# Performance work log

Hardware: AMD Instinct MI355X
Metric: run time of the kernel (lower is better)

Reference implementation:

```python
import jax, jax.numpy as jnp
import numpy as np

D_MODEL = 1024
D_INNER = 2048      # expand * d_model
D_STATE = 64
HEADDIM = 128
NHEADS = 16         # d_inner // headdim
D_CONV = 4
CHUNK = 256
D_IN_PROJ = 2 * D_INNER + 2 * D_STATE + NHEADS   # 4240 (ngroups=1)
CONV_DIM = D_INNER + 2 * D_STATE                 # 2176
EPS = 1e-5


def setup_inputs() -> dict:
    key = jax.random.key(0)
    ks = jax.random.split(key, 8)
    B, L = 2, 4096
    u = jax.random.normal(ks[0], (B, L, D_MODEL), jnp.float32)
    in_proj_w = jax.random.normal(ks[1], (D_IN_PROJ, D_MODEL), jnp.float32) / np.sqrt(D_MODEL)
    conv_w = jax.random.uniform(ks[2], (CONV_DIM, D_CONV), jnp.float32, -0.5, 0.5)
    conv_b = jnp.zeros((CONV_DIM,), jnp.float32)
    # dt_bias init exactly as in the module: inv-softplus of dt ~ logU(1e-3, 1e-1)
    dt0 = jnp.exp(jax.random.uniform(ks[3], (NHEADS,), jnp.float32) * (np.log(0.1) - np.log(0.001)) + np.log(0.001))
    dt_bias = dt0 + jnp.log(-jnp.expm1(-dt0))
    A_log = jnp.log(jax.random.uniform(ks[4], (NHEADS,), jnp.float32, 1.0, 16.0))
    Dp = jnp.ones((NHEADS,), jnp.float32)
    norm_w = jnp.ones((D_INNER,), jnp.float32)
    out_proj_w = jax.random.normal(ks[5], (D_MODEL, D_INNER), jnp.float32) / np.sqrt(D_INNER)
    return dict(u=u, in_proj_w=in_proj_w, conv_w=conv_w, conv_b=conv_b, dt_bias=dt_bias,
                A_log=A_log, Dp=Dp, norm_w=norm_w, out_proj_w=out_proj_w)


def _ssd(x, dt, A, Bm, Cm, Dp):
    # Chunked selective state-space scan (mamba_chunk_scan_combined semantics).
    # x: [b,l,h,p], dt: [b,l,h] (already softplus'd), A: [h] (negative), Bm/Cm: [b,l,n]
    b, l, h, p = x.shape
    n = Bm.shape[-1]
    nc = l // CHUNK
    xc = x.reshape(b, nc, CHUNK, h, p)
    dtc = dt.reshape(b, nc, CHUNK, h)
    Bc = Bm.reshape(b, nc, CHUNK, n)
    Cc = Cm.reshape(b, nc, CHUNK, n)
    a = dtc * A                       # [b,c,q,h], a <= 0
    acum = jnp.cumsum(a, axis=2)      # within-chunk cumulative log-decay
    # ---- intra-chunk (causal, attention-like) ----
    scores = jnp.einsum('bcqn,bckn->bcqk', Cc, Bc)
    diff = acum[:, :, :, None, :] - acum[:, :, None, :, :]        # [b,c,q,k,h]
    mask = jnp.tril(jnp.ones((CHUNK, CHUNK), bool))[None, None, :, :, None]
    decay = jnp.exp(jnp.where(mask, diff, -jnp.inf))
    M = scores[..., None] * decay * dtc[:, :, None, :, :]         # [b,c,q,k,h]
    y_diag = jnp.einsum('bcqkh,bckhp->bcqhp', M, xc)
    # ---- per-chunk end states ----
    decay_states = jnp.exp(acum[:, :, -1:, :] - acum)             # [b,c,q,h]
    states = jnp.einsum('bcqh,bcqn,bcqhp->bchpn', dtc * decay_states, Bc, xc)
    # ---- inter-chunk recurrence (scan over nc chunks) ----
    chunk_decay = jnp.exp(acum[:, :, -1, :])                      # [b,c,h]
    def step(s, inp):
        st, cd = inp
        return cd[:, :, None, None] * s + st, s                   # emit state BEFORE this chunk
    init = jnp.zeros((b, h, p, n), x.dtype)
    _, prev = jax.lax.scan(step, init, (states.transpose(1, 0, 2, 3, 4), chunk_decay.transpose(1, 0, 2)))
    prev = prev.transpose(1, 0, 2, 3, 4)                          # [b,c,h,p,n]
    y_off = jnp.einsum('bcqn,bchpn,bcqh->bcqhp', Cc, prev, jnp.exp(acum))
    y = y_diag + y_off + xc * Dp[None, None, None, :, None]
    return y.reshape(b, l, h, p)


def _forward(u, in_proj_w, conv_w, conv_b, dt_bias, A_log, Dp, norm_w, out_proj_w):
    b, l, _ = u.shape
    zxbct = jnp.einsum('bld,ed->ble', u, in_proj_w)
    z = zxbct[..., :D_INNER]
    xBC = zxbct[..., D_INNER:D_INNER + CONV_DIM]
    dt = zxbct[..., D_INNER + CONV_DIM:]
    dt = jax.nn.softplus(dt + dt_bias)                            # [b,l,h]
    # causal depthwise conv1d (padding d_conv-1, truncated to seq_len) + SiLU
    xp = jnp.pad(xBC, ((0, 0), (D_CONV - 1, 0), (0, 0)))
    conv_out = conv_b
    for w in range(D_CONV):
        conv_out = conv_out + xp[:, w:w + l, :] * conv_w[:, w]
    xBC = jax.nn.silu(conv_out)
    x = xBC[..., :D_INNER]
    Bm = xBC[..., D_INNER:D_INNER + D_STATE]
    Cm = xBC[..., D_INNER + D_STATE:]
    A = -jnp.exp(A_log)
    y = _ssd(x.reshape(b, l, NHEADS, HEADDIM), dt, A, Bm, Cm, Dp)
    y = y.reshape(b, l, D_INNER)
    # RMSNormGated (norm_before_gate=False): gate first, then RMSNorm
    y = y * jax.nn.silu(z)
    y = y * jax.lax.rsqrt(jnp.mean(y * y, axis=-1, keepdims=True) + EPS) * norm_w
    return jnp.einsum('ble,de->bld', y, out_proj_w)


def reference(u, in_proj_w, conv_w, conv_b, dt_bias, A_log, Dp, norm_w, out_proj_w):
    return _forward(u, in_proj_w, conv_w, conv_b, dt_bias, A_log, Dp, norm_w, out_proj_w)
```

## Files before the change

kernel.cpp:

```cpp
#include <hip/hip_runtime.h>
#include <hip/hip_bf16.h>
#include <cstdint>
#include <cstddef>

#define D_MODEL   1024
#define D_INNER   2048
#define D_STATE   64
#define HEADDIM   128
#define NHEADS    16
#define D_CONV    4
#define CHUNK     256
#define D_IN_PROJ 4240
#define ZPAD      4352
#define CONV_DIM  2176
#define NB        2
#define LEN       4096
#define NC        16
#define MROWS     (NB*LEN)

typedef __hip_bfloat16 bf16;
typedef __bf16 bf16x8 __attribute__((ext_vector_type(8)));
typedef float  f32x4  __attribute__((ext_vector_type(4)));
typedef unsigned short us4 __attribute__((ext_vector_type(4)));

__device__ __forceinline__ float fsilu(float x){ return x / (1.f + __expf(-x)); }
__device__ __forceinline__ float toF(float x){ return x; }
__device__ __forceinline__ float toF(bf16 x){ return __bfloat162float(x); }
__device__ __forceinline__ void storeF(float* p, float v){ *p = v; }
__device__ __forceinline__ void storeF(bf16* p, float v){ *p = __float2bfloat16(v); }

__device__ __forceinline__ unsigned short f2bs(float v){
  return __bfloat16_as_ushort(__float2bfloat16(v));
}
__device__ __forceinline__ void store4(bf16* p, f32x4 v){
  us4 o; o[0]=f2bs(v[0]); o[1]=f2bs(v[1]); o[2]=f2bs(v[2]); o[3]=f2bs(v[3]);
  *(us4*)p = o;
}
__device__ __forceinline__ void store4(float* p, f32x4 v){
  *(f32x4*)p = v;
}

__device__ __forceinline__ void gload_lds16(const void* g, void* l){
  __builtin_amdgcn_global_load_lds(
     (const __attribute__((address_space(1))) unsigned int*)(uintptr_t)g,
     (__attribute__((address_space(3))) unsigned int*)(uintptr_t)l, 16, 0, 0);
}

template<typename TC>
__global__ __launch_bounds__(512) void k_gemm_pipe(
    const bf16* __restrict__ A, int lda,
    const bf16* __restrict__ B, int ldb,
    TC* __restrict__ C, int ldc, int K)
{
  __shared__ __align__(16) char lds[3*49152];
  const int tid  = threadIdx.x;
  const int w    = tid >> 6, l = tid & 63;
  const int quad = l >> 4, lq = l & 15;
  const int wm   = w >> 1, wn = w & 1;

  const int nwg  = gridDim.x;
  const int orig = blockIdx.x;
  const int wg   = (orig & 7)*(nwg >> 3) + (orig >> 3);
  const int m0   = (wg & 31)*256;
  const int n0   = (wg >> 5)*128;

  const int rs = tid >> 3;
  const int cs = ((tid & 7) ^ (rs & 7)) * 8;
  const bf16* Ag = A + (size_t)(m0 + rs)*lda + cs;
  const bf16* Bg = B + (size_t)(n0 + rs)*ldb + cs;
  const int sdo = w*1024;

  auto stage = [&](int k0, char* bufb){
    #pragma unroll
    for (int p=0;p<4;p++)
      gload_lds16(Ag + (size_t)p*64*lda + k0, bufb + sdo + p*8192);
    #pragma unroll
    for (int p=0;p<2;p++)
      gload_lds16(Bg + (size_t)p*64*ldb + k0, bufb + 32768 + sdo + p*8192);
  };

  char* bufA = lds;
  char* bufB = lds + 49152;
  char* bufC = lds + 98304;

  f32x4 acc[4][4] = {};
  const int sl0 = (quad ^ (lq & 7)) * 16;
  const int sl1 = sl0 ^ 64;
  const int aro = (wm*64 + lq)*128;
  const int bro = 32768 + (wn*64 + lq)*128;

  stage(0,  bufA);
  stage(64, bufB);
  asm volatile("s_waitcnt vmcnt(6)" ::: "memory");
  __builtin_amdgcn_s_barrier();
  asm volatile("" ::: "memory");

  const int NT = K >> 6;
  for (int t = 0; t < NT; ++t){
    if (t + 2 < NT) stage((t+2) << 6, bufC);

    bf16x8 af[2][4], bfr[2][4];
    #pragma unroll
    for (int m=0;m<4;m++){
      af[0][m]  = *(const bf16x8*)(bufA + aro + m*2048 + sl0);
      af[1][m]  = *(const bf16x8*)(bufA + aro + m*2048 + sl1);
      bfr[0][m] = *(const bf16x8*)(bufA + bro + m*2048 + sl0);
      bfr[1][m] = *(const bf16x8*)(bufA + bro + m*2048 + sl1);
    }
    __builtin_amdgcn_s_setprio(1);
    #pragma unroll
    for (int ks=0;ks<2;ks++)
      #pragma unroll
      for (int m=0;m<4;m++)
        #pragma unroll
        for (int n=0;n<4;n++)
          acc[m][n] = __builtin_amdgcn_mfma_f32_16x16x32_bf16(bfr[ks][n], af[ks][m], acc[m][n], 0,0,0);
    __builtin_amdgcn_s_setprio(0);

    __builtin_amdgcn_sched_barrier(0);
    if (t == NT-2) { asm volatile("s_waitcnt vmcnt(0)" ::: "memory"); }
    else           { asm volatile("s_waitcnt vmcnt(6)" ::: "memory"); }
    __builtin_amdgcn_s_barrier();
    asm volatile("" ::: "memory");
    char* tmp = bufA; bufA = bufB; bufB = bufC; bufC = tmp;
  }

  #pragma unroll
  for (int m=0;m<4;m++){
    const int r = m0 + wm*64 + m*16 + lq;
    #pragma unroll
    for (int n=0;n<4;n++){
      const int cb = n0 + wn*64 + n*16 + quad*4;
      store4(&C[(size_t)r*ldc + cb], acc[m][n]);
    }
  }
}

#define NU4  (MROWS*D_MODEL/4)
#define NW14 (ZPAD*D_MODEL/4)
#define NW24 (D_MODEL*D_INNER/4)
__global__ __launch_bounds__(256) void k_convert(
    const float* __restrict__ u, const float* __restrict__ Win,
    const float* __restrict__ Wout, const float* __restrict__ norm_w,
    bf16* __restrict__ ub, bf16* __restrict__ Wb_in, bf16* __restrict__ Wb_out){
  int i4 = blockIdx.x*256 + threadIdx.x;
  if (i4 < NU4){
    float4 v = ((const float4*)u)[i4];
    us4 o = {f2bs(v.x), f2bs(v.y), f2bs(v.z), f2bs(v.w)};
    ((us4*)ub)[i4] = o;
  } else if (i4 < NU4 + NW14){
    int j = i4 - NU4;
    int r = j >> 8;
    float4 v = make_float4(0.f,0.f,0.f,0.f);
    if (r < D_IN_PROJ) v = ((const float4*)Win)[j];
    us4 o = {f2bs(v.x), f2bs(v.y), f2bs(v.z), f2bs(v.w)};
    ((us4*)Wb_in)[j] = o;
  } else {
    int j = i4 - NU4 - NW14;
    float4 v = ((const float4*)Wout)[j];
    float4 nw = ((const float4*)norm_w)[j & 511];
    us4 o = {f2bs(v.x*nw.x), f2bs(v.y*nw.y), f2bs(v.z*nw.z), f2bs(v.w*nw.w)};
    ((us4*)Wb_out)[j] = o;
  }
}

__global__ __launch_bounds__(256) void k_dt(
    const bf16* __restrict__ zxbct, const float* __restrict__ dt_bias,
    const float* __restrict__ A_log, float* __restrict__ dt_t,
    float* __restrict__ acum_t, float* __restrict__ cd_t){
  int bid = blockIdx.x;
  int h = bid & 15, c = (bid>>4)&15, b = bid>>8;
  int q = threadIdx.x;
  size_t m = (size_t)(b*NC + c)*CHUNK + q;
  float x = toF(zxbct[m*ZPAD + (D_INNER + CONV_DIM) + h]) + dt_bias[h];
  float dtv = (x > 20.f) ? x : log1pf(__expf(x));
  float Ah = -__expf(A_log[h]);
  float a = dtv * Ah;
  __shared__ float sb[CHUNK];
  sb[q] = a;
  __syncthreads();
  #pragma unroll
  for (int off=1; off<CHUNK; off<<=1){
    float t = (q >= off) ? sb[q-off] : 0.f;
    __syncthreads();
    sb[q] += t;
    __syncthreads();
  }
  float ac = sb[q];
  size_t o = ((size_t)(b*NHEADS+h))*LEN + c*CHUNK + q;
  dt_t[o]   = dtv;
  acum_t[o] = ac;
  if (q == CHUNK-1) cd_t[(b*NHEADS+h)*NC + c] = __expf(ac);
}

__global__ __launch_bounds__(256) void k_conv(
    const bf16* __restrict__ zxbct, const float* __restrict__ conv_w,
    const float* __restrict__ conv_b, bf16* __restrict__ xbc){
  __shared__ __align__(16) __bf16 xs[67*64];
  __shared__ __align__(16) float  ws[64*4];
  __shared__ float bs[64];
  const int tid = threadIdx.x;
  const int cq = tid & 7;
  const int tm = tid >> 3;
  const int c0 = blockIdx.x*64;
  const int m0 = blockIdx.y*64;
  {
    int g = m0 - 3 + tm; if (g < 0) g = 0;
    *(bf16x8*)&xs[tm*64 + cq*8] =
        *(const bf16x8*)(zxbct + (size_t)g*ZPAD + D_INNER + c0 + cq*8);
    int g2 = m0 - 3 + tm + 32;
    *(bf16x8*)&xs[(tm+32)*64 + cq*8] =
        *(const bf16x8*)(zxbct + (size_t)g2*ZPAD + D_INNER + c0 + cq*8);
    if (tid < 24){
      int r3 = 64 + (tid >> 3);
      int g3 = m0 - 3 + r3;
      *(bf16x8*)&xs[r3*64 + cq*8] =
          *(const bf16x8*)(zxbct + (size_t)g3*ZPAD + D_INNER + c0 + cq*8);
    }
  }
  if (tid < 64)      *(float4*)&ws[tid*4] = *(const float4*)(conv_w + (size_t)(c0+tid)*4);
  else if (tid < 128) bs[tid-64] = conv_b[c0 + tid - 64];
  __syncthreads();

  #pragma unroll
  for (int rr=0; rr<2; rr++){
    const int r = tm + rr*32;
    const int m = m0 + r;
    const int l = m & (LEN-1);
    float acc[8];
    #pragma unroll
    for (int j=0;j<8;j++) acc[j] = bs[cq*8+j];
    #pragma unroll
    for (int w=0; w<D_CONV; w++){
      if (l - (D_CONV-1) + w >= 0){
        bf16x8 v = *(const bf16x8*)&xs[(r+w)*64 + cq*8];
        #pragma unroll
        for (int j=0;j<8;j++) acc[j] += (float)v[j] * ws[(cq*8+j)*4 + w];
      }
    }
    bf16x8 o;
    #pragma unroll
    for (int j=0;j<8;j++) o[j] = (__bf16)fsilu(acc[j]);
    *(bf16x8*)(xbc + (size_t)m*CONV_DIM + c0 + cq*8) = o;
  }
}

__global__ __launch_bounds__(256,2) void k_states(
    const bf16* __restrict__ xbc, const float* __restrict__ acum_t,
    const float* __restrict__ dt_t, float* __restrict__ states)
{
  const int bid = blockIdx.x;
  const int h = bid & 15, c = (bid>>4)&15, b = bid>>8;
  const int z = b*NC + c;
  const int tid = threadIdx.x;
  const int w = tid >> 6, l = tid & 63;
  const int quad = l >> 4, lq = l & 15;

  __shared__ __align__(16) __bf16 xsT[2][128*72];
  __shared__ __align__(16) __bf16 bts[2][64*72];

  const float* acum = acum_t + ((size_t)(b*NHEADS+h))*LEN + c*CHUNK;
  const float* dtc  = dt_t   + ((size_t)(b*NHEADS+h))*LEN + c*CHUNK;
  const float alast = acum[CHUNK-1];
  const bf16* xrow = xbc + (size_t)z*CHUNK*CONV_DIM + h*HEADDIM;
  const bf16* Brow = xbc + (size_t)z*CHUNK*CONV_DIM + D_INNER;

  f32x4 Sst[2][4] = {};

  auto stage = [&](int t, int buf){
    const int k0 = t*64;
    const bf16* xr = xrow + (size_t)(k0+l)*CONV_DIM;
    #pragma unroll
    for (int pass=0; pass<4; pass++){
      int pb = w*8 + pass*32;
      bf16x8 v = *(const bf16x8*)(xr + pb);
      #pragma unroll
      for (int j=0;j<8;j++) xsT[buf][(pb+j)*72 + l] = v[j];
    }
    float wl = dtc[k0+l] * __expf(alast - acum[k0+l]);
    const bf16* br = Brow + (size_t)(k0+l)*CONV_DIM;
    #pragma unroll
    for (int pass=0; pass<2; pass++){
      int nb = w*8 + pass*32;
      bf16x8 v = *(const bf16x8*)(br + nb);
      #pragma unroll
      for (int j=0;j<8;j++) bts[buf][(nb+j)*72 + l] = (__bf16)((float)v[j] * wl);
    }
  };

  stage(0, 0);
  for (int t = 0; t < 4; t++){
    const int buf = t & 1;
    __syncthreads();
    if (t < 3) stage(t+1, buf^1);
    #pragma unroll
    for (int s=0;s<2;s++){
      bf16x8 a2[2];
      #pragma unroll
      for (int mi=0;mi<2;mi++)
        a2[mi] = *(const bf16x8*)&xsT[buf][(w*32 + mi*16 + lq)*72 + s*32 + quad*8];
      #pragma unroll
      for (int ni=0;ni<4;ni++){
        bf16x8 bb = *(const bf16x8*)&bts[buf][(ni*16+lq)*72 + s*32 + quad*8];
        #pragma unroll
        for (int mi=0;mi<2;mi++)
          Sst[mi][ni] = __builtin_amdgcn_mfma_f32_16x16x32_bf16(bb, a2[mi], Sst[mi][ni], 0,0,0);
      }
    }
  }

  float* so = states + (size_t)bid*HEADDIM*D_STATE;
  #pragma unroll
  for (int mi=0;mi<2;mi++){
    int pp = w*32 + mi*16 + lq;
    #pragma unroll
    for (int ni=0;ni<4;ni++)
      store4(&so[pp*D_STATE + ni*16 + quad*4], Sst[mi][ni]);
  }
}

__global__ __launch_bounds__(256) void k_scan(
    const float* __restrict__ states, const float* __restrict__ cd_t,
    bf16* __restrict__ prevb){
  int b = blockIdx.x >> 4, h = blockIdx.x & 15;
  int pt = blockIdx.y;
  int tid = threadIdx.x;
  float carry[4] = {0.f,0.f,0.f,0.f};
  for (int c=0;c<NC;c++){
    size_t base = ((size_t)(b*256 + c*16 + h))*HEADDIM*D_STATE + (size_t)pt*1024;
    float cd = cd_t[(b*NHEADS+h)*NC + c];
    #pragma unroll
    for (int i=0;i<4;i++){
      size_t idx = base + (size_t)i*256 + tid;
      prevb[idx] = __float2bfloat16(carry[i]);
      carry[i] = carry[i]*cd + states[idx];
    }
  }
}

__global__ __launch_bounds__(256,2) void k_fused(
    const bf16* __restrict__ xbc, const float* __restrict__ acum_t,
    const float* __restrict__ dt_t, const float* __restrict__ Dp,
    const bf16* __restrict__ prevb, bf16* __restrict__ y)
{
  const int bid = blockIdx.x;
  const int h = bid & 15, c = (bid>>4)&15, b = bid>>8;
  const int z = b*NC + c;
  const int tid = threadIdx.x;
  const int w = tid >> 6, l = tid & 63;
  const int quad = l >> 4, lq = l & 15;

  __shared__ __align__(16) __bf16 xsT[2][128*72];
  __shared__ __align__(16) __bf16 Ms[4][32*40];
  __shared__ float acs[CHUNK], dts[CHUNK];

  const float* acum = acum_t + ((size_t)(b*NHEADS+h))*LEN + c*CHUNK;
  const float* dtc  = dt_t   + ((size_t)(b*NHEADS+h))*LEN + c*CHUNK;
  acs[tid] = acum[tid];
  dts[tid] = dtc[tid];

  const bf16* xrow = xbc + (size_t)z*CHUNK*CONV_DIM + h*HEADDIM;
  const bf16* Brow = xbc + (size_t)z*CHUNK*CONV_DIM + D_INNER;
  const bf16* Crow = xbc + (size_t)z*CHUNK*CONV_DIM + D_INNER + D_STATE;
  const bf16* pv   = prevb + (size_t)bid*HEADDIM*D_STATE;
  const float Dph = Dp[h];
  const int j0 = w, j1 = 7 - w;

  f32x4 Yacc[2][2][8] = {};

  auto stage = [&](int t, int buf){
    const bf16* xr = xrow + (size_t)(t*64+l)*CONV_DIM;
    #pragma unroll
    for (int pass=0; pass<4; pass++){
      int pb = w*8 + pass*32;
      bf16x8 v = *(const bf16x8*)(xr + pb);
      #pragma unroll
      for (int j=0;j<8;j++) xsT[buf][(pb+j)*72 + l] = v[j];
    }
  };

  stage(0, 0);
  __syncthreads();

  #pragma unroll
  for (int s=0;s<2;s++){
    bf16x8 bp[8];
    #pragma unroll
    for (int pn=0;pn<8;pn++)
      bp[pn] = *(const bf16x8*)(pv + (pn*16+lq)*D_STATE + s*32 + quad*8);
    #pragma unroll
    for (int half=0; half<2; half++){
      const int j = half ? j1 : j0;
      #pragma unroll
      for (int qm=0;qm<2;qm++){
        int row = j*32 + qm*16 + lq;
        float e = __expf(acs[row]);
        bf16x8 a = *(const bf16x8*)(Crow + (size_t)row*CONV_DIM + s*32 + quad*8);
        bf16x8 ae;
        #pragma unroll
        for (int jj=0;jj<8;jj++) ae[jj] = (__bf16)((float)a[jj] * e);
        #pragma unroll
        for (int pn=0;pn<8;pn++)
          Yacc[half][qm][pn] = __builtin_amdgcn_mfma_f32_16x16x32_bf16(bp[pn], ae, Yacc[half][qm][pn], 0,0,0);
      }
    }
  }

  for (int t = 0; t < 4; t++){
    const int buf = t & 1;
    if (t > 0) __syncthreads();
    if (t < 3) stage(t+1, buf^1);

    #pragma unroll
    for (int half=0; half<2; half++){
      const int j = half ? j1 : j0;
      if (2*t > j) continue;
      const int qbase = j*32;
      bf16x8 cf[2][2];
      #pragma unroll
      for (int s=0;s<2;s++)
        #pragma unroll
        for (int qm=0;qm<2;qm++)
          cf[s][qm] = *(const bf16x8*)(Crow + (size_t)(qbase+qm*16+lq)*CONV_DIM + s*32 + quad*8);
      #pragma unroll
      for (int kk=0; kk<2; kk++){
        const int kh = 2*t + kk;
        if (kh > j) continue;
        const int kb32  = kk*32;
        const int kbase = kh*32;
        f32x4 Sacc[2][2] = {};
        #pragma unroll
        for (int s=0;s<2;s++){
          bf16x8 bfk[2];
          #pragma unroll
          for (int kn=0;kn<2;kn++)
            bfk[kn] = *(const bf16x8*)(Brow + (size_t)(kbase+kn*16+lq)*CONV_DIM + s*32 + quad*8);
          #pragma unroll
          for (int kn=0;kn<2;kn++)
            #pragma unroll
            for (int qm=0;qm<2;qm++)
              Sacc[kn][qm] = __builtin_amdgcn_mfma_f32_16x16x32_bf16(bfk[kn], cf[s][qm], Sacc[kn][qm], 0,0,0);
        }
        #pragma unroll
        for (int qm=0;qm<2;qm++){
          int ql = qbase + qm*16 + lq;
          float aq = acs[ql];
          #pragma unroll
          for (int kn=0;kn<2;kn++){
            us4 o;
            #pragma unroll
            for (int i=0;i<4;i++){
              int kl = kbase + kn*16 + quad*4 + i;
              float v = Sacc[kn][qm][i] * __expf(aq - acs[kl]) * dts[kl];
              v = (kl < ql) ? v : ((kl == ql) ? v + Dph : 0.f);
              o[i] = f2bs(v);
            }
            *(us4*)&Ms[w][(qm*16+lq)*40 + kn*16 + quad*4] = o;
          }
        }
        asm volatile("s_waitcnt lgkmcnt(0)" ::: "memory");
        #pragma unroll
        for (int qm=0;qm<2;qm++){
          bf16x8 am = *(const bf16x8*)&Ms[w][(qm*16+lq)*40 + quad*8];
          #pragma unroll
          for (int pn=0;pn<8;pn++){
            bf16x8 bp = *(const bf16x8*)&xsT[buf][(pn*16+lq)*72 + kb32 + quad*8];
            Yacc[half][qm][pn] = __builtin_amdgcn_mfma_f32_16x16x32_bf16(bp, am, Yacc[half][qm][pn], 0,0,0);
          }
        }
      }
    }
  }

  bf16* yrow = y + (size_t)z*CHUNK*D_INNER + h*HEADDIM;
  #pragma unroll
  for (int half=0; half<2; half++){
    const int j = half ? j1 : j0;
    #pragma unroll
    for (int qm=0;qm<2;qm++){
      int q = j*32 + qm*16 + lq;
      #pragma unroll
      for (int pn=0;pn<8;pn++)
        store4(&yrow[(size_t)q*D_INNER + pn*16 + quad*4], Yacc[half][qm][pn]);
    }
  }
}

__global__ __launch_bounds__(256) void k_gatenorm(
    const bf16* __restrict__ zxbct, bf16* __restrict__ y){
  int m = blockIdx.x;
  int e0 = threadIdx.x*8;
  bf16x8 zv = *(const bf16x8*)(zxbct + (size_t)m*ZPAD + e0);
  bf16x8 yv = *(const bf16x8*)(y + (size_t)m*D_INNER + e0);
  float v[8]; float ss = 0.f;
  #pragma unroll
  for (int j=0;j<8;j++){
    float val = (float)yv[j] * fsilu((float)zv[j]);
    v[j] = val; ss += val*val;
  }
  #pragma unroll
  for (int off=32; off>0; off>>=1) ss += __shfl_down(ss, off, 64);
  __shared__ float red[4];
  if ((threadIdx.x & 63) == 0) red[threadIdx.x >> 6] = ss;
  __syncthreads();
  float tot = red[0]+red[1]+red[2]+red[3];
  float r = rsqrtf(tot * (1.f/D_INNER) + 1e-5f);
  bf16x8 o;
  #pragma unroll
  for (int j=0;j<8;j++) o[j] = (__bf16)(v[j] * r);
  *(bf16x8*)(y + (size_t)m*D_INNER + e0) = o;
}

extern "C" void kernel_launch(void* const* d_in, const int* in_sizes, int n_in,
                              void* d_out, int out_size, void* d_ws, size_t ws_size,
                              hipStream_t stream) {
  const float* u         = (const float*)d_in[0];
  const float* in_proj_w = (const float*)d_in[1];
  const float* conv_w    = (const float*)d_in[2];
  const float* conv_b    = (const float*)d_in[3];
  const float* dt_bias   = (const float*)d_in[4];
  const float* A_log     = (const float*)d_in[5];
  const float* Dp        = (const float*)d_in[6];
  const float* norm_w    = (const float*)d_in[7];
  const float* out_proj_w= (const float*)d_in[8];
  float* out = (float*)d_out;

  char* p = (char*)d_ws;
  auto alloc = [&](size_t bytes){ char* r = p; p += (bytes + 255) & ~size_t(255); return r; };
  bf16*  zxbct = (bf16*) alloc((size_t)MROWS*ZPAD*2);
  bf16*  xbc   = (bf16*) alloc((size_t)MROWS*CONV_DIM*2);
  bf16*  y     = (bf16*) alloc((size_t)MROWS*D_INNER*2);
  bf16*  ub    = (bf16*) alloc((size_t)MROWS*D_MODEL*2);
  bf16*  Wb_in = (bf16*) alloc((size_t)ZPAD*D_MODEL*2);
  bf16*  Wb_out= (bf16*) alloc((size_t)D_MODEL*D_INNER*2);
  float* dt_t  = (float*)alloc((size_t)NB*NHEADS*LEN*4);
  float* acum_t= (float*)alloc((size_t)NB*NHEADS*LEN*4);
  float* cd_t  = (float*)alloc((size_t)NB*NHEADS*NC*4);
  float* states= (float*)ub;
  bf16*  prevb = (bf16*)Wb_in;

  dim3 blk(256);
  k_convert<<<dim3((NU4+NW14+NW24)/256), blk, 0, stream>>>(
      u, in_proj_w, out_proj_w, norm_w, ub, Wb_in, Wb_out);

  k_gemm_pipe<bf16><<<dim3(32*34), dim3(512), 0, stream>>>(
      ub, D_MODEL, Wb_in, D_MODEL, zxbct, ZPAD, D_MODEL);

  k_dt    <<<dim3(NB*NC*NHEADS), blk, 0, stream>>>(zxbct, dt_bias, A_log, dt_t, acum_t, cd_t);
  k_conv  <<<dim3(CONV_DIM/64, MROWS/64), blk, 0, stream>>>(zxbct, conv_w, conv_b, xbc);
  k_states<<<dim3(NB*NC*NHEADS), blk, 0, stream>>>(xbc, acum_t, dt_t, states);
  k_scan  <<<dim3(NB*NHEADS, 8), blk, 0, stream>>>(states, cd_t, prevb);
  k_fused <<<dim3(NB*NC*NHEADS), blk, 0, stream>>>(xbc, acum_t, dt_t, Dp, prevb, y);
  k_gatenorm<<<dim3(MROWS), blk, 0, stream>>>(zxbct, y);

  k_gemm_pipe<float><<<dim3(32*8), dim3(512), 0, stream>>>(
      y, D_INNER, Wb_out, D_INNER, out, D_MODEL, D_INNER);
}
```

Baseline: 386.1 us.

## Restructure GEMM to 4 waves with 128x64 warp tiles and K=32 stages

The pipelined bf16 GEMM moves from 512 threads (8 waves, 64x64 per wave, 64-wide K stages) to 256 threads (4 waves, 128x64 per wave, 32-wide K stages), with launch bounds allowing two blocks per CU. It also drops the XCD-aware block remapping in favour of a plain 2D grid, and skips the final barrier. The aim is more register-level reuse per wave and a smaller LDS footprint so two workgroups can share a CU. The costs are higher register pressure from 32 accumulators per lane, twice as many loop iterations and barriers, and possibly worse L2 locality without the swizzle.

Result: faster. 362.7 us (-6.1%).

```diff
diff --git a/kernel.cpp b/kernel.cpp
--- a/kernel.cpp
+++ b/kernel.cpp
@@ -47,25 +47,21 @@
 }
 
 template<typename TC>
-__global__ __launch_bounds__(512) void k_gemm_pipe(
+__global__ __launch_bounds__(256, 2) void k_gemm_pipe(
     const bf16* __restrict__ A, int lda,
     const bf16* __restrict__ B, int ldb,
     TC* __restrict__ C, int ldc, int K)
 {
-  __shared__ __align__(16) char lds[3*49152];
+  __shared__ __align__(16) char lds[3*24576];
   const int tid  = threadIdx.x;
   const int w    = tid >> 6, l = tid & 63;
   const int quad = l >> 4, lq = l & 15;
-  const int wm   = w >> 1, wn = w & 1;
-
-  const int nwg  = gridDim.x;
-  const int orig = blockIdx.x;
-  const int wg   = (orig & 7)*(nwg >> 3) + (orig >> 3);
-  const int m0   = (wg & 31)*256;
-  const int n0   = (wg >> 5)*128;
-
-  const int rs = tid >> 3;
-  const int cs = ((tid & 7) ^ (rs & 7)) * 8;
+  const int wm   = (w >> 1)*128, wn = (w & 1)*64;
+
+  const int m0 = blockIdx.x*256, n0 = blockIdx.y*128;
+
+  const int rs = tid >> 2;
+  const int cs = ((tid & 3) ^ (rs & 3)) * 8;
   const bf16* Ag = A + (size_t)(m0 + rs)*lda + cs;
   const bf16* Bg = B + (size_t)(n0 + rs)*ldb + cs;
   const int sdo = w*1024;
@@ -73,64 +69,61 @@
   auto stage = [&](int k0, char* bufb){
     #pragma unroll
     for (int p=0;p<4;p++)
-      gload_lds16(Ag + (size_t)p*64*lda + k0, bufb + sdo + p*8192);
+      gload_lds16(Ag + (size_t)p*64*lda + k0, bufb + p*4096 + sdo);
     #pragma unroll
     for (int p=0;p<2;p++)
-      gload_lds16(Bg + (size_t)p*64*ldb + k0, bufb + 32768 + sdo + p*8192);
+      gload_lds16(Bg + (size_t)p*64*ldb + k0, bufb + 16384 + p*4096 + sdo);
   };
 
   char* bufA = lds;
-  char* bufB = lds + 49152;
-  char* bufC = lds + 98304;
-
-  f32x4 acc[4][4] = {};
-  const int sl0 = (quad ^ (lq & 7)) * 16;
-  const int sl1 = sl0 ^ 64;
-  const int aro = (wm*64 + lq)*128;
-  const int bro = 32768 + (wn*64 + lq)*128;
+  char* bufB = lds + 24576;
+  char* bufC = lds + 49152;
+
+  f32x4 acc[8][4] = {};
+  const int sl  = (quad ^ (lq & 3)) * 16;
+  const int aro = (wm + lq)*64;
+  const int bro = 16384 + (wn + lq)*64;
 
   stage(0,  bufA);
-  stage(64, bufB);
+  stage(32, bufB);
   asm volatile("s_waitcnt vmcnt(6)" ::: "memory");
   __builtin_amdgcn_s_barrier();
   asm volatile("" ::: "memory");
 
-  const int NT = K >> 6;
+  const int NT = K >> 5;
   for (int t = 0; t < NT; ++t){
-    if (t + 2 < NT) stage((t+2) << 6, bufC);
-
-    bf16x8 af[2][4], bfr[2][4];
-    #pragma unroll
-    for (int m=0;m<4;m++){
-      af[0][m]  = *(const bf16x8*)(bufA + aro + m*2048 + sl0);
-      af[1][m]  = *(const bf16x8*)(bufA + aro + m*2048 + sl1);
-      bfr[0][m] = *(const bf16x8*)(bufA + bro + m*2048 + sl0);
-      bfr[1][m] = *(const bf16x8*)(bufA + bro + m*2048 + sl1);
-    }
+    if (t + 2 < NT) stage((t+2) << 5, bufC);
+
+    bf16x8 af[8], bfr[4];
+    #pragma unroll
+    for (int m=0;m<8;m++) af[m]  = *(const bf16x8*)(bufA + aro + m*1024 + sl);
+    #pragma unroll
+    for (int n=0;n<4;n++) bfr[n] = *(const bf16x8*)(bufA + bro + n*1024 + sl);
+
     __builtin_amdgcn_s_setprio(1);
     #pragma unroll
-    for (int ks=0;ks<2;ks++)
-      #pragma unroll
-      for (int m=0;m<4;m++)
-        #pragma unroll
-        for (int n=0;n<4;n++)
-          acc[m][n] = __builtin_amdgcn_mfma_f32_16x16x32_bf16(bfr[ks][n], af[ks][m], acc[m][n], 0,0,0);
+    for (int m=0;m<8;m++)
+      #pragma unroll
+      for (int n=0;n<4;n++)
+        acc[m][n] = __builtin_amdgcn_mfma_f32_16x16x32_bf16(bfr[n], af[m], acc[m][n], 0,0,0);
     __builtin_amdgcn_s_setprio(0);
 
-    __builtin_amdgcn_sched_barrier(0);
-    if (t == NT-2) { asm volatile("s_waitcnt vmcnt(0)" ::: "memory"); }
-    else           { asm volatile("s_waitcnt vmcnt(6)" ::: "memory"); }
-    __builtin_amdgcn_s_barrier();
-    asm volatile("" ::: "memory");
+    if (t < NT-1){
+      __builtin_amdgcn_sched_barrier(0);
+      if (t == NT-2) { asm volatile("s_waitcnt vmcnt(0)" ::: "memory"); }
+      else           { asm volatile("s_waitcnt vmcnt(6)" ::: "memory"); }
+      __builtin_amdgcn_s_barrier();
+      asm volatile("" ::: "memory");
+    }
     char* tmp = bufA; bufA = bufB; bufB = bufC; bufC = tmp;
   }
 
   #pragma unroll
-  for (int m=0;m<4;m++){
-    const int r = m0 + wm*64 + m*16 + lq;
+  for (int m=0;m<8;m++){
+    const int r = m0 + wm + m*16 + lq;
     #pragma unroll
     for (int n=0;n<4;n++){
-      const int cb = n0 + wn*64 + n*16 + quad*4;
+      const int cb = n0 + wn + n*16 + quad*4;
       store4(&C[(size_t)r*ldc + cb], acc[m][n]);
     }
   }
@@ -543,7 +536,7 @@
   k_convert<<<dim3((NU4+NW14+NW24)/256), blk, 0, stream>>>(
       u, in_proj_w, out_proj_w, norm_w, ub, Wb_in, Wb_out);
 
-  k_gemm_pipe<bf16><<<dim3(32*34), dim3(512), 0, stream>>>(
+  k_gemm_pipe<bf16><<<dim3(32, 34), dim3(256), 0, stream>>>(
       ub, D_MODEL, Wb_in, D_MODEL, zxbct, ZPAD, D_MODEL);
 
   k_dt    <<<dim3(NB*NC*NHEADS), blk, 0, stream>>>(zxbct, dt_bias, A_log, dt_t, acum_t, cd_t);
@@ -553,6 +546,6 @@
   k_fused <<<dim3(NB*NC*NHEADS), blk, 0, stream>>>(xbc, acum_t, dt_t, Dp, prevb, y);
   k_gatenorm<<<dim3(MROWS), blk, 0, stream>>>(zxbct, y);
 
-  k_gemm_pipe<float><<<dim3(32*8), dim3(512), 0, stream>>>(
+  k_gemm_pipe<float><<<dim3(32, 8), dim3(256), 0, stream>>>(
       y, D_INNER, Wb_out, D_INNER, out, D_MODEL, D_INNER);
 }
```
